# Optimization experiments

Hardware: AMD Instinct MI355X
Metric: run time of the kernel (lower is better)

## Reference

```python
import jax, jax.numpy as jnp
import numpy as np


def gcn_conv(x, edge_index, edge_weight, W, b):
    """PyG GCNConv: add self-loops (weight 1), symmetric normalization,
    linear transform, edge-weighted scatter-add aggregation, bias."""
    N = x.shape[0]
    src = jnp.concatenate([edge_index[0], jnp.arange(N, dtype=edge_index.dtype)])
    dst = jnp.concatenate([edge_index[1], jnp.arange(N, dtype=edge_index.dtype)])
    ew = jnp.concatenate([edge_weight, jnp.ones((N,), dtype=edge_weight.dtype)])
    # deg over destination nodes (source_to_target flow)
    deg = jax.ops.segment_sum(ew, dst, num_segments=N)
    dinv = jnp.where(deg > 0, deg ** -0.5, 0.0).astype(x.dtype)
    norm = dinv[src] * ew * dinv[dst]          # [E+N]
    xw = x @ W                                  # [N, out] linear first (cheaper)
    msgs = norm[:, None] * xw[src]              # [E+N, out]
    out = jax.ops.segment_sum(msgs, dst, num_segments=N)
    return out + b


def setup_inputs() -> dict:
    key = jax.random.key(0)
    ks = jax.random.split(key, 7)
    N, E, F_in, H, F_out = 100000, 1600000, 394, 256, 64
    x = jax.random.normal(ks[0], (N, F_in), dtype=jnp.float32)
    edge_index = jax.random.randint(ks[1], (2, E), 0, N, dtype=jnp.int32)
    edge_weight = jax.random.uniform(ks[2], (E,), dtype=jnp.float32)
    W1 = jax.random.normal(ks[3], (F_in, H), dtype=jnp.float32) * (1.0 / np.sqrt(F_in))
    b1 = jnp.zeros((H,), dtype=jnp.float32)
    W2 = jax.random.normal(ks[4], (H, F_out), dtype=jnp.float32) * (1.0 / np.sqrt(H))
    b2 = jnp.zeros((F_out,), dtype=jnp.float32)
    return {"x": x, "edge_index": edge_index, "edge_weight": edge_weight,
            "W1": W1, "b1": b1, "W2": W2, "b2": b2}


def reference(x, edge_index, edge_weight, W1, b1, W2, b2):
    h = gcn_conv(x, edge_index, edge_weight, W1, b1)
    h = jax.nn.relu(h)
    # F.dropout(training=self.training) is identity in eval mode
    out = gcn_conv(h, edge_index, edge_weight, W2, b2)
    return out
```

## Files before the change

kernel.cpp:

```cpp
#include <hip/hip_runtime.h>
#include <hip/hip_bf16.h>
#include <hip/hip_fp16.h>
#include <type_traits>


typedef _Float16 f16x8 __attribute__((ext_vector_type(8)));
typedef float f32x4 __attribute__((ext_vector_type(4)));

#define DEG_MASK ((1ull << 42) - 1)

__device__ inline void async_copy16(const void* g, void* l) {
    __builtin_amdgcn_global_load_lds(
        (const __attribute__((address_space(1))) void*)g,
        (__attribute__((address_space(3))) void*)l, 16, 0, 0);
}


__global__ __launch_bounds__(256) void init_node(unsigned long long* packed, int N) {
    int i = blockIdx.x * 256 + threadIdx.x;
    if (i < N) packed[i] = 0ull;
}

__global__ __launch_bounds__(256) void accum_deg_hist(const int* __restrict__ dst,
                                                      const float* __restrict__ ew,
                                                      unsigned long long* packed, int E) {
    int e = blockIdx.x * 256 + threadIdx.x;
    if (e < E) {
        int d = dst[e];
        unsigned long long add =
            (1ull << 42) + (unsigned long long)(ew[e] * 4294967296.0f);
        atomicAdd(&packed[d], add);
    }
}

#define SCAN_TILE 2048

__global__ __launch_bounds__(256) void scan1(const unsigned long long* __restrict__ packed,
                                             int* __restrict__ rowptr,
                                             float* __restrict__ dinv,
                                             int* __restrict__ bsums, int N) {
    __shared__ int tmp[256];
    int t = threadIdx.x;
    int base = blockIdx.x * SCAN_TILE + t * 8;
    int v[8], s = 0;
#pragma unroll
    for (int j = 0; j < 8; ++j) {
        int idx = base + j;
        if (idx < N) {
            unsigned long long pv = packed[idx];
            v[j] = (int)(pv >> 42);
            dinv[idx] = rsqrtf(1.0f + (float)(pv & DEG_MASK) * (1.0f / 4294967296.0f));
        } else v[j] = 0;
        s += v[j];
    }
    tmp[t] = s;
    __syncthreads();
#pragma unroll
    for (int off = 1; off < 256; off <<= 1) {
        int u = (t >= off) ? tmp[t - off] : 0;
        __syncthreads();
        tmp[t] += u;
        __syncthreads();
    }
    int run = tmp[t] - s;
#pragma unroll
    for (int j = 0; j < 8; ++j) {
        if (base + j < N) rowptr[base + j] = run;
        run += v[j];
    }
    if (t == 255) bsums[blockIdx.x] = tmp[255];
}

__global__ __launch_bounds__(256) void scan2(int* bsums, int* rowptr, int NB, int N, int E) {
    __shared__ int tmp[256];
    int t = threadIdx.x;
    int v = (t < NB) ? bsums[t] : 0;
    tmp[t] = v;
    __syncthreads();
#pragma unroll
    for (int off = 1; off < 256; off <<= 1) {
        int u = (t >= off) ? tmp[t - off] : 0;
        __syncthreads();
        tmp[t] += u;
        __syncthreads();
    }
    if (t < NB) bsums[t] = tmp[t] - v;
    if (t == 0) rowptr[N] = E;
}

__global__ __launch_bounds__(256) void scan3(int* rowptr, int* cursor,
                                             const int* __restrict__ bsums, int N) {
    int base = blockIdx.x * SCAN_TILE + threadIdx.x * 8;
    int off = bsums[blockIdx.x];
#pragma unroll
    for (int j = 0; j < 8; ++j)
        if (base + j < N) {
            int v = rowptr[base + j] + off;
            rowptr[base + j] = v;
            cursor[base + j] = v;
        }
}

__global__ __launch_bounds__(256) void fill_csr(const int* __restrict__ src,
                                                const int* __restrict__ dst,
                                                const float* __restrict__ ew,
                                                const float* __restrict__ dinv,
                                                int* __restrict__ cursor,
                                                int2* __restrict__ cv, int E) {
    int e = blockIdx.x * 256 + threadIdx.x;
    if (e < E) {
        int d = dst[e], s = src[e];
        int pos = atomicAdd(&cursor[d], 1);
        float v = dinv[s] * ew[e] * dinv[d];
        cv[pos] = make_int2(s, __float_as_int(v));
    }
}

__global__ __launch_bounds__(256) void tohalf_w(const float* __restrict__ W,
                                                __half* __restrict__ WT,
                                                int K, int N, int Kpad) {
    int idx = blockIdx.x * 256 + threadIdx.x;
    int total = N * Kpad;
    if (idx >= total) return;
    int n = idx / Kpad, k = idx % Kpad;
    float v = (k < K) ? W[(size_t)k * N + n] : 0.0f;
    WT[idx] = __float2half(v);
}

template <int BM, int BN, int WARPS_M, int WARPS_N, int NT>
__global__ __launch_bounds__(NT) void gemm_f32a(const float* __restrict__ Ax,
                                                const __half* __restrict__ BT,
                                                __half* __restrict__ C,
                                                int M, int K, int Kpad) {
    const int WM = BM / WARPS_M, WN = BN / WARPS_N;
    const int FM = WM / 16, FN = WN / 16;
    const int ACH = BM * 4;
    const int BCH = BN * 4;
    static_assert(ACH == NT, "1 A-chunk per thread");
    static_assert(BCH == 2 * NT, "2 B-chunks per thread");
    __shared__ __align__(16) __half lds[2][(ACH + BCH) * 8];

    int tid = threadIdx.x;
    int lane = tid & 63;
    int w = tid >> 6;
    int wr = w / WARPS_N, wc = w % WARPS_N;
    int bm = blockIdx.x * BM;
    int lrow = lane & 15;
    int lslot = lane >> 4;

    int arow = tid >> 2, ap = tid & 3;
    int aslot = ap ^ ((arow >> 1) & 3);
    int agrow = bm + arow; if (agrow >= M) agrow = M - 1;
    const float* abase = Ax + (size_t)agrow * K;

    const __half* bsrc[2];
#pragma unroll
    for (int i = 0; i < 2; ++i) {
        int c = tid + i * NT;
        int row = c >> 2, p = c & 3;
        bsrc[i] = BT + (size_t)row * Kpad + (size_t)((p ^ ((row >> 1) & 3)) * 8);
    }

    f32x4 acc[FM][FN];
#pragma unroll
    for (int m = 0; m < FM; ++m)
#pragma unroll
        for (int n = 0; n < FN; ++n) acc[m][n] = (f32x4){0.f, 0.f, 0.f, 0.f};

    float2 ar[4];
    auto loadA = [&](int s) {
        int gk = s * 32 + aslot * 8;
        if (gk + 8 <= K) {
            const float* p = abase + gk;
            ar[0] = *(const float2*)p;
            ar[1] = *(const float2*)(p + 2);
            ar[2] = *(const float2*)(p + 4);
            ar[3] = *(const float2*)(p + 6);
        } else {
            float t[8];
#pragma unroll
            for (int j = 0; j < 8; ++j) t[j] = (gk + j < K) ? abase[gk + j] : 0.0f;
            ar[0] = make_float2(t[0], t[1]);
            ar[1] = make_float2(t[2], t[3]);
            ar[2] = make_float2(t[4], t[5]);
            ar[3] = make_float2(t[6], t[7]);
        }
    };
    auto writeA = [&](int buf) {
        union { __half2 h[4]; uint4 u; } pk;
#pragma unroll
        for (int j = 0; j < 4; ++j) pk.h[j] = __floats2half2_rn(ar[j].x, ar[j].y);
        *(uint4*)&lds[buf][(size_t)tid * 8] = pk.u;
    };
    auto stageB = [&](int buf) {
#pragma unroll
        for (int i = 0; i < 2; ++i) {
            async_copy16(bsrc[i], &lds[buf][(size_t)((tid & ~63) + (i + 1) * NT) * 8]);
            bsrc[i] += 32;
        }
    };

    auto compute = [&](int buf) {
        f16x8 af[FM], bf[FN];
#pragma unroll
        for (int m = 0; m < FM; ++m) {
            int row = wr * WM + m * 16 + lrow;
            int p = lslot ^ ((row >> 1) & 3);
            af[m] = *(const f16x8*)&lds[buf][(size_t)(row * 4 + p) * 8];
        }
#pragma unroll
        for (int n = 0; n < FN; ++n) {
            int row = wc * WN + n * 16 + lrow;
            int p = lslot ^ ((row >> 1) & 3);
            bf[n] = *(const f16x8*)&lds[buf][(size_t)(ACH + row * 4 + p) * 8];
        }
#pragma unroll
        for (int m = 0; m < FM; ++m)
#pragma unroll
            for (int n = 0; n < FN; ++n)
                acc[m][n] = __builtin_amdgcn_mfma_f32_16x16x32_f16(af[m], bf[n], acc[m][n], 0, 0, 0);
    };

    const int nsteps = Kpad / 32;
    loadA(0);
    stageB(0);
    asm volatile("s_waitcnt vmcnt(2)" ::: "memory");
    writeA(0);
    asm volatile("s_waitcnt vmcnt(0) lgkmcnt(0)" ::: "memory");
    __builtin_amdgcn_s_barrier();
    for (int s = 0; s < nsteps; ++s) {
        bool more = (s + 1 < nsteps);
        if (more) { loadA(s + 1); stageB((s + 1) & 1); }
        compute(s & 1);
        if (more) {
            asm volatile("s_waitcnt vmcnt(2)" ::: "memory");
            writeA((s + 1) & 1);
            asm volatile("s_waitcnt vmcnt(0) lgkmcnt(0)" ::: "memory");
        }
        __builtin_amdgcn_s_barrier();
    }

    __syncthreads();
    {
        const int LW = WN + 8;
        __half* tile = (__half*)lds + (size_t)w * 16 * LW;
        const int CPR = WN / 8;
        const int CHT = (16 * CPR) / 64;
#pragma unroll
        for (int m = 0; m < FM; ++m) {
            int rb = bm + wr * WM + m * 16;
#pragma unroll
            for (int n = 0; n < FN; ++n)
#pragma unroll
                for (int i = 0; i < 4; ++i)
                    tile[((lane >> 4) * 4 + i) * LW + n * 16 + (lane & 15)] =
                        __float2half(acc[m][n][i]);
#pragma unroll
            for (int c = 0; c < CHT; ++c) {
                int ch = lane + c * 64;
                int r = ch / CPR, cc = ch % CPR;
                uint4 v = *(uint4*)&tile[r * LW + cc * 8];
                int grow = rb + r;
                if (grow < M)
                    *(uint4*)&C[(size_t)grow * BN + wc * WN + cc * 8] = v;
            }
        }
    }
}

template <int BM, int BN, int WARPS_M, int WARPS_N, int NT>
__global__ __launch_bounds__(NT) void gemm_f16(const __half* __restrict__ Ah,
                                               const __half* __restrict__ BT,
                                               __half* __restrict__ C,
                                               int M, int Kpad) {
    const int WM = BM / WARPS_M, WN = BN / WARPS_N;
    const int FM = WM / 16, FN = WN / 16;
    const int ACH = BM * 4;
    const int BCH = BN * 4;
    const int TOTCH = ACH + BCH;
    const int CH = TOTCH / NT;
    static_assert(CH == 3, "vmcnt(3) hardcoded below");
    __shared__ __align__(16) __half lds[2][TOTCH * 8];

    int tid = threadIdx.x;
    int lane = tid & 63;
    int w = tid >> 6;
    int wr = w / WARPS_N, wc = w % WARPS_N;
    int bm = blockIdx.x * BM;
    int lrow = lane & 15;
    int lslot = lane >> 4;

    const __half* srcp[CH];
#pragma unroll
    for (int i = 0; i < CH; ++i) {
        int ch = tid + i * NT;
        if (ch < ACH) {
            int c = ch, row = c >> 2;
            int grow = bm + row;
            if (grow >= M) grow = M - 1;
            srcp[i] = Ah + (size_t)grow * Kpad + (size_t)(((c & 3) ^ ((row >> 1) & 3)) * 8);
        } else {
            int c = ch - ACH, row = c >> 2;
            srcp[i] = BT + (size_t)row * Kpad + (size_t)(((c & 3) ^ ((row >> 1) & 3)) * 8);
        }
    }

    f32x4 acc[FM][FN];
#pragma unroll
    for (int m = 0; m < FM; ++m)
#pragma unroll
        for (int n = 0; n < FN; ++n) acc[m][n] = (f32x4){0.f, 0.f, 0.f, 0.f};

    auto stage = [&](int buf) {
#pragma unroll
        for (int i = 0; i < CH; ++i) {
            async_copy16(srcp[i], &lds[buf][(size_t)((tid & ~63) + i * NT) * 8]);
            srcp[i] += 32;
        }
    };

    auto compute = [&](int buf) {
        f16x8 af[FM], bf[FN];
#pragma unroll
        for (int m = 0; m < FM; ++m) {
            int row = wr * WM + m * 16 + lrow;
            int p = lslot ^ ((row >> 1) & 3);
            af[m] = *(const f16x8*)&lds[buf][(size_t)(row * 4 + p) * 8];
        }
#pragma unroll
        for (int n = 0; n < FN; ++n) {
            int row = wc * WN + n * 16 + lrow;
            int p = lslot ^ ((row >> 1) & 3);
            bf[n] = *(const f16x8*)&lds[buf][(size_t)(ACH + row * 4 + p) * 8];
        }
#pragma unroll
        for (int m = 0; m < FM; ++m)
#pragma unroll
            for (int n = 0; n < FN; ++n)
                acc[m][n] = __builtin_amdgcn_mfma_f32_16x16x32_f16(af[m], bf[n], acc[m][n], 0, 0, 0);
    };

    const int nsteps = Kpad / 32;
    stage(0);
    for (int s = 0; s < nsteps; ++s) {
        if (s + 1 < nsteps) {
            stage((s + 1) & 1);
            asm volatile("s_waitcnt vmcnt(3)" ::: "memory");
        } else {
            asm volatile("s_waitcnt vmcnt(0)" ::: "memory");
        }
        __builtin_amdgcn_s_barrier();
        compute(s & 1);
        __builtin_amdgcn_s_barrier();
    }

    __syncthreads();
    {
        const int LW = WN + 8;
        __half* tile = (__half*)lds + (size_t)w * 16 * LW;
        const int CPR = WN / 8;
        const int CHT = (16 * CPR) / 64;
#pragma unroll
        for (int m = 0; m < FM; ++m) {
            int rb = bm + wr * WM + m * 16;
#pragma unroll
            for (int n = 0; n < FN; ++n)
#pragma unroll
                for (int i = 0; i < 4; ++i)
                    tile[((lane >> 4) * 4 + i) * LW + n * 16 + (lane & 15)] =
                        __float2half(acc[m][n][i]);
#pragma unroll
            for (int c = 0; c < CHT; ++c) {
                int ch = lane + c * 64;
                int r = ch / CPR, cc = ch % CPR;
                uint4 v = *(uint4*)&tile[r * LW + cc * 8];
                int grow = rb + r;
                if (grow < M)
                    *(uint4*)&C[(size_t)grow * BN + wc * WN + cc * 8] = v;
            }
        }
    }
}

template <int F, int LPN, int RELU, typename OutT>
__global__ __launch_bounds__(256) void gatherh(const int* __restrict__ rowptr,
                                               const int2* __restrict__ cv,
                                               const __half* __restrict__ xw,
                                               const float* __restrict__ dinv,
                                               const float* __restrict__ bias,
                                               OutT* __restrict__ out, int N) {
    const int NPB = 256 / LPN;
    int d = blockIdx.x * NPB + threadIdx.x / LPN;
    if (d >= N) return;
    int lane = threadIdx.x % LPN;

    float di = dinv[d];
    float w = di * di;
    uint2 raw = *(const uint2*)(xw + (size_t)d * F + lane * 4);
    float2 u0 = __half22float2(*(__half2*)&raw.x);
    float2 u1 = __half22float2(*(__half2*)&raw.y);
    float a0 = w * u0.x, a1 = w * u0.y, a2 = w * u1.x, a3 = w * u1.y;
    float b0 = 0.f, b1 = 0.f, b2 = 0.f, b3 = 0.f;

    int p = rowptr[d], p1 = rowptr[d + 1];
    for (; p + 4 <= p1; p += 4) {
        int2 e0 = cv[p], e1 = cv[p + 1], e2 = cv[p + 2], e3 = cv[p + 3];
        uint2 r0 = *(const uint2*)(xw + (size_t)e0.x * F + lane * 4);
        uint2 r1 = *(const uint2*)(xw + (size_t)e1.x * F + lane * 4);
        uint2 r2 = *(const uint2*)(xw + (size_t)e2.x * F + lane * 4);
        uint2 r3 = *(const uint2*)(xw + (size_t)e3.x * F + lane * 4);
        float w0 = __int_as_float(e0.y), w1 = __int_as_float(e1.y);
        float w2 = __int_as_float(e2.y), w3 = __int_as_float(e3.y);
        {
            float2 v0 = __half22float2(*(__half2*)&r0.x);
            float2 v1 = __half22float2(*(__half2*)&r0.y);
            a0 = fmaf(w0, v0.x, a0); a1 = fmaf(w0, v0.y, a1);
            a2 = fmaf(w0, v1.x, a2); a3 = fmaf(w0, v1.y, a3);
        }
        {
            float2 v0 = __half22float2(*(__half2*)&r1.x);
            float2 v1 = __half22float2(*(__half2*)&r1.y);
            b0 = fmaf(w1, v0.x, b0); b1 = fmaf(w1, v0.y, b1);
            b2 = fmaf(w1, v1.x, b2); b3 = fmaf(w1, v1.y, b3);
        }
        {
            float2 v0 = __half22float2(*(__half2*)&r2.x);
            float2 v1 = __half22float2(*(__half2*)&r2.y);
            a0 = fmaf(w2, v0.x, a0); a1 = fmaf(w2, v0.y, a1);
            a2 = fmaf(w2, v1.x, a2); a3 = fmaf(w2, v1.y, a3);
        }
        {
            float2 v0 = __half22float2(*(__half2*)&r3.x);
            float2 v1 = __half22float2(*(__half2*)&r3.y);
            b0 = fmaf(w3, v0.x, b0); b1 = fmaf(w3, v0.y, b1);
            b2 = fmaf(w3, v1.x, b2); b3 = fmaf(w3, v1.y, b3);
        }
    }
    for (; p < p1; ++p) {
        int2 e = cv[p];
        float wv = __int_as_float(e.y);
        uint2 rv = *(const uint2*)(xw + (size_t)e.x * F + lane * 4);
        float2 v0 = __half22float2(*(__half2*)&rv.x);
        float2 v1 = __half22float2(*(__half2*)&rv.y);
        a0 = fmaf(wv, v0.x, a0); a1 = fmaf(wv, v0.y, a1);
        a2 = fmaf(wv, v1.x, a2); a3 = fmaf(wv, v1.y, a3);
    }
    a0 += b0; a1 += b1; a2 += b2; a3 += b3;

    float4 bb = *(const float4*)&bias[lane * 4];
    a0 += bb.x; a1 += bb.y; a2 += bb.z; a3 += bb.w;
    if (RELU) {
        a0 = fmaxf(a0, 0.f); a1 = fmaxf(a1, 0.f);
        a2 = fmaxf(a2, 0.f); a3 = fmaxf(a3, 0.f);
    }
    if constexpr (std::is_same_v<OutT, float>) {
        *(float4*)&out[(size_t)d * F + lane * 4] = make_float4(a0, a1, a2, a3);
    } else {
        __half2 h0 = __floats2half2_rn(a0, a1);
        __half2 h1 = __floats2half2_rn(a2, a3);
        uint2 packed;
        packed.x = *(uint*)&h0;
        packed.y = *(uint*)&h1;
        *(uint2*)&out[(size_t)d * F + lane * 4] = packed;
    }
}

extern "C" void kernel_launch(void* const* d_in, const int* in_sizes, int n_in,
                              void* d_out, int out_size, void* d_ws, size_t ws_size,
                              hipStream_t stream) {
    const float* x  = (const float*)d_in[0];
    const int*   ei = (const int*)d_in[1];
    const float* ew = (const float*)d_in[2];
    const float* W1 = (const float*)d_in[3];
    const float* b1 = (const float*)d_in[4];
    const float* W2 = (const float*)d_in[5];
    const float* b2 = (const float*)d_in[6];
    float* out = (float*)d_out;

    const int H    = in_sizes[4];
    const int Fout = in_sizes[6];
    const int Fin  = in_sizes[3] / H;
    const int N    = in_sizes[0] / Fin;
    const int E    = in_sizes[2];

    const int Kpad1 = (Fin + 31) / 32 * 32;
    const int Kpad2 = (H + 31) / 32 * 32;

    const int* src = ei;
    const int* dst = ei + E;

    unsigned long long* packed = (unsigned long long*)d_ws;
    float* dinv   = (float*)(packed + N);
    int*   rowptr = (int*)(dinv + N);
    int*   cursor = rowptr + N + 4;
    int*   bsums  = cursor + N + 4;
    int2*  cv     = (int2*)(bsums + 256);
    __half* bufA  = (__half*)(cv + E);
    __half* bufB  = bufA + (size_t)N * H;
    __half* wt1   = bufB + (size_t)N * H;
    __half* wt2   = wt1 + (size_t)H * Kpad1;

    const int NB = (N + SCAN_TILE - 1) / SCAN_TILE;

    init_node<<<(N + 255) / 256, 256, 0, stream>>>(packed, N);
    accum_deg_hist<<<(E + 255) / 256, 256, 0, stream>>>(dst, ew, packed, E);

    scan1<<<NB, 256, 0, stream>>>(packed, rowptr, dinv, bsums, N);
    scan2<<<1, 256, 0, stream>>>(bsums, rowptr, NB, N, E);
    scan3<<<NB, 256, 0, stream>>>(rowptr, cursor, bsums, N);
    fill_csr<<<(E + 255) / 256, 256, 0, stream>>>(src, dst, ew, dinv, cursor, cv, E);

    tohalf_w<<<(H * Kpad1 + 255) / 256, 256, 0, stream>>>(W1, wt1, Fin, H, Kpad1);
    tohalf_w<<<(Fout * Kpad2 + 255) / 256, 256, 0, stream>>>(W2, wt2, H, Fout, Kpad2);

    gemm_f32a<128, 256, 2, 4, 512><<<(N + 127) / 128, 512, 0, stream>>>(
        x, wt1, bufA, N, Fin, Kpad1);

    gatherh<256, 64, 1, __half><<<(N + 3) / 4, 256, 0, stream>>>(
        rowptr, cv, bufA, dinv, b1, bufB, N);

    gemm_f16<128, 64, 2, 2, 256><<<(N + 127) / 128, 256, 0, stream>>>(bufB, wt2, bufA, N, Kpad2);

    gatherh<64, 16, 0, float><<<(N + 15) / 16, 256, 0, stream>>>(
        rowptr, cv, bufA, dinv, b2, out, N);
}
```

Baseline: 466.8 us.

## Prefetch GEMM A two stages ahead and factor dinv[d] out of aggregation

The GEMM main loop now double-buffers the A-operand registers so global loads for step s+2 are issued before computing step s, giving the fp32 A loads more latency slack. The loop is unrolled by two to alternate the register sets, and the vmcnt waits are adjusted to match. The K-tail load becomes branchless by clamping the address and zeroing out-of-range values. Separately, the destination dinv is removed from the per-edge CSR weight and applied once per node after the sum, saving a multiply and a load per edge in fill_csr, at the cost of higher register pressure in the GEMM.

Result: slower. 494.2 us (+5.9%).

```diff
diff --git a/kernel.cpp b/kernel.cpp
--- a/kernel.cpp
+++ b/kernel.cpp
@@ -111,7 +111,7 @@
     if (e < E) {
         int d = dst[e], s = src[e];
         int pos = atomicAdd(&cursor[d], 1);
-        float v = dinv[s] * ew[e] * dinv[d];
+        float v = dinv[s] * ew[e];
         cv[pos] = make_int2(s, __float_as_int(v));
     }
 }
@@ -167,26 +167,20 @@
 #pragma unroll
         for (int n = 0; n < FN; ++n) acc[m][n] = (f32x4){0.f, 0.f, 0.f, 0.f};
 
-    float2 ar[4];
-    auto loadA = [&](int s) {
+    float2 arA[4], arB[4];
+
+    auto loadA = [&](int s, float2 (&ar)[4]) {
         int gk = s * 32 + aslot * 8;
-        if (gk + 8 <= K) {
-            const float* p = abase + gk;
-            ar[0] = *(const float2*)p;
-            ar[1] = *(const float2*)(p + 2);
-            ar[2] = *(const float2*)(p + 4);
-            ar[3] = *(const float2*)(p + 6);
-        } else {
-            float t[8];
-#pragma unroll
-            for (int j = 0; j < 8; ++j) t[j] = (gk + j < K) ? abase[gk + j] : 0.0f;
-            ar[0] = make_float2(t[0], t[1]);
-            ar[1] = make_float2(t[2], t[3]);
-            ar[2] = make_float2(t[4], t[5]);
-            ar[3] = make_float2(t[6], t[7]);
-        }
-    };
-    auto writeA = [&](int buf) {
+#pragma unroll
+        for (int j = 0; j < 4; ++j) {
+            int kk = gk + 2 * j;
+            int ck = (kk <= K - 2) ? kk : (K - 2);
+            float2 v = *(const float2*)(abase + ck);
+            if (kk >= K) { v.x = 0.0f; v.y = 0.0f; }
+            ar[j] = v;
+        }
+    };
+    auto writeA = [&](int buf, float2 (&ar)[4]) {
         union { __half2 h[4]; uint4 u; } pk;
 #pragma unroll
         for (int j = 0; j < 4; ++j) pk.h[j] = __floats2half2_rn(ar[j].x, ar[j].y);
@@ -222,23 +216,36 @@
     };
 
     const int nsteps = Kpad / 32;
-    loadA(0);
+    loadA(0, arA);
     stageB(0);
-    asm volatile("s_waitcnt vmcnt(2)" ::: "memory");
-    writeA(0);
-    asm volatile("s_waitcnt vmcnt(0) lgkmcnt(0)" ::: "memory");
+    loadA(1, arB);
+    asm volatile("s_waitcnt vmcnt(6)" ::: "memory");
+    writeA(0, arA);
+    asm volatile("s_waitcnt vmcnt(4)" ::: "memory");
+    asm volatile("s_waitcnt lgkmcnt(0)" ::: "memory");
     __builtin_amdgcn_s_barrier();
-    for (int s = 0; s < nsteps; ++s) {
-        bool more = (s + 1 < nsteps);
-        if (more) { loadA(s + 1); stageB((s + 1) & 1); }
+
+    auto iter = [&](int s, float2 (&wset)[4], float2 (&lset)[4]) {
+        bool m1 = (s + 1 < nsteps), m2 = (s + 2 < nsteps);
+        if (m1) stageB((s + 1) & 1);
+        if (m2) loadA(s + 2, lset);
         compute(s & 1);
-        if (more) {
-            asm volatile("s_waitcnt vmcnt(2)" ::: "memory");
-            writeA((s + 1) & 1);
-            asm volatile("s_waitcnt vmcnt(0) lgkmcnt(0)" ::: "memory");
+        if (m1) {
+            if (m2) asm volatile("s_waitcnt vmcnt(6)" ::: "memory");
+            else    asm volatile("s_waitcnt vmcnt(2)" ::: "memory");
+            writeA((s + 1) & 1, wset);
+            if (m2) asm volatile("s_waitcnt vmcnt(4)" ::: "memory");
+            else    asm volatile("s_waitcnt vmcnt(0)" ::: "memory");
+            asm volatile("s_waitcnt lgkmcnt(0)" ::: "memory");
         }
         __builtin_amdgcn_s_barrier();
-    }
+    };
+    int s = 0;
+    for (; s + 1 < nsteps; s += 2) {
+        iter(s, arB, arA);
+        iter(s + 1, arA, arB);
+    }
+    if (s < nsteps) iter(s, arB, arA);
 
     __syncthreads();
     {
@@ -395,11 +402,10 @@
     int lane = threadIdx.x % LPN;
 
     float di = dinv[d];
-    float w = di * di;
     uint2 raw = *(const uint2*)(xw + (size_t)d * F + lane * 4);
     float2 u0 = __half22float2(*(__half2*)&raw.x);
     float2 u1 = __half22float2(*(__half2*)&raw.y);
-    float a0 = w * u0.x, a1 = w * u0.y, a2 = w * u1.x, a3 = w * u1.y;
+    float a0 = di * u0.x, a1 = di * u0.y, a2 = di * u1.x, a3 = di * u1.y;
     float b0 = 0.f, b1 = 0.f, b2 = 0.f, b3 = 0.f;
 
     int p = rowptr[d], p1 = rowptr[d + 1];
@@ -446,6 +452,7 @@
         a2 = fmaf(wv, v1.x, a2); a3 = fmaf(wv, v1.y, a3);
     }
     a0 += b0; a1 += b1; a2 += b2; a3 += b3;
+    a0 *= di; a1 *= di; a2 *= di; a3 *= di;
 
     float4 bb = *(const float4*)&bias[lane * 4];
     a0 += bb.x; a1 += bb.y; a2 += bb.z; a3 += bb.w;
```
